# Performance work log

Measured on AMD Instinct MI355X. Metric: run time of the kernel, lower is better.

The kernel has to match this reference:

```python
import jax, jax.numpy as jnp
import numpy as np

HIDDEN = 2048
N_HEADS = 16
N_KV_HEADS = 4
HEAD_DIM = HIDDEN // N_HEADS  # 128
BATCH = 2
SEQ = 2048


def setup_inputs() -> dict:
    key = jax.random.key(0)
    ks = jax.random.split(key, 10)
    s = 0.02
    return {
        "hidden_states": jax.random.normal(ks[0], (BATCH, SEQ, HIDDEN), jnp.float32),
        "attention_mask": jnp.ones((BATCH, SEQ), jnp.int32),
        # weights stored [in, out] so y = x @ W + b (transpose of torch layout)
        "Wq": jax.random.normal(ks[1], (HIDDEN, N_HEADS * HEAD_DIM), jnp.float32) * s,
        "bq": jnp.zeros((N_HEADS * HEAD_DIM,), jnp.float32),
        "Wk": jax.random.normal(ks[2], (HIDDEN, N_KV_HEADS * HEAD_DIM), jnp.float32) * s,
        "bk": jnp.zeros((N_KV_HEADS * HEAD_DIM,), jnp.float32),
        "Wv": jax.random.normal(ks[3], (HIDDEN, N_KV_HEADS * HEAD_DIM), jnp.float32) * s,
        "bv": jnp.zeros((N_KV_HEADS * HEAD_DIM,), jnp.float32),
        "Wo": jax.random.normal(ks[4], (N_HEADS * HEAD_DIM, HIDDEN), jnp.float32) * s,
        "bo": jnp.zeros((HIDDEN,), jnp.float32),
    }


def reference(hidden_states, attention_mask, Wq, bq, Wk, bk, Wv, bv, Wo, bo):
    B, S, _ = hidden_states.shape
    q = hidden_states @ Wq + bq  # [B,S,H*D]
    k = hidden_states @ Wk + bk  # [B,S,Hkv*D]
    v = hidden_states @ Wv + bv

    q = q.reshape(B, S, N_HEADS, HEAD_DIM).transpose(0, 2, 1, 3)      # [B,H,S,D]
    k = k.reshape(B, S, N_KV_HEADS, HEAD_DIM).transpose(0, 2, 1, 3)   # [B,Hkv,S,D]
    v = v.reshape(B, S, N_KV_HEADS, HEAD_DIM).transpose(0, 2, 1, 3)

    # GQA: repeat_interleave along head dim (head h uses kv head h // groups)
    groups = N_HEADS // N_KV_HEADS
    k = jnp.repeat(k, groups, axis=1)  # [B,H,S,D]
    v = jnp.repeat(v, groups, axis=1)

    scale = 1.0 / np.sqrt(HEAD_DIM)
    scores = jnp.einsum('bhqd,bhkd->bhqk', q, k) * scale  # [B,H,S,S]

    causal = jnp.tril(jnp.ones((S, S), bool))              # True = keep
    keep = causal[None, None, :, :] & (attention_mask[:, None, None, :] != 0)
    scores = jnp.where(keep, scores, -jnp.inf)

    attn = jax.nn.softmax(scores.astype(jnp.float32), axis=-1).astype(q.dtype)
    out = jnp.einsum('bhqk,bhkd->bhqd', attn, v)            # [B,H,S,D]
    out = out.transpose(0, 2, 1, 3).reshape(B, S, N_HEADS * HEAD_DIM)
    return out @ Wo + bo
```

## Files before the change

### kernel.cpp

```cpp
#include <hip/hip_runtime.h>
#include <hip/hip_bf16.h>


typedef unsigned short u16;
typedef __attribute__((ext_vector_type(8))) short short8;
typedef __attribute__((ext_vector_type(4))) float f32x4;

#define BATCH 2
#define SEQ 2048
#define HIDDEN 2048
#define NH 16
#define NKV 4
#define HD 128
#define QKV_N 3072
#define MROWS 4096

__device__ inline u16 f2bf(float f) {
    __hip_bfloat16 h = __float2bfloat16(f);
    return __builtin_bit_cast(u16, h);
}

__device__ inline void async_copy16(const u16* g, u16* lds_base) {
    __builtin_amdgcn_global_load_lds(
        (const __attribute__((address_space(1))) void*)g,
        (__attribute__((address_space(3))) void*)lds_base, 16, 0, 0);
}

__global__ void convert_f32_bf16(const float* __restrict__ src, u16* __restrict__ dst, int n) {
    int i = (blockIdx.x * 256 + threadIdx.x) * 4;
    if (i + 3 < n) {
        float4 v = *(const float4*)(src + i);
        ushort4 o;
        o.x = f2bf(v.x); o.y = f2bf(v.y); o.z = f2bf(v.z); o.w = f2bf(v.w);
        *(ushort4*)(dst + i) = o;
    }
}

__global__ void transpose_f32_bf16(const float* __restrict__ src, u16* __restrict__ dst,
                                   int K, int N) {
    __shared__ float tile[32][33];
    int n0 = blockIdx.x * 32, k0 = blockIdx.y * 32;
    int tx = threadIdx.x, ty = threadIdx.y;
#pragma unroll
    for (int i = 0; i < 32; i += 8)
        tile[ty + i][tx] = src[(size_t)(k0 + ty + i) * N + n0 + tx];
    __syncthreads();
#pragma unroll
    for (int i = 0; i < 32; i += 8)
        dst[(size_t)(n0 + ty + i) * K + k0 + tx] = f2bf(tile[tx][ty + i]);
}

__global__ void build_bias(const float* __restrict__ bq, const float* __restrict__ bk,
                           const float* __restrict__ bv, float* __restrict__ bqkv) {
    int i = blockIdx.x * 256 + threadIdx.x;
    if (i < QKV_N)
        bqkv[i] = (i < 2048) ? bq[i] : ((i < 2560) ? bk[i - 2048] : bv[i - 2560]);
}

__global__ void vt_from_qkv(const u16* __restrict__ qkv, u16* __restrict__ vt) {
    __shared__ u16 tile[32][33];
    int b = blockIdx.z >> 2, kvh = blockIdx.z & 3;
    int s0 = blockIdx.x * 32, d0 = blockIdx.y * 32;
    int tx = threadIdx.x, ty = threadIdx.y;
#pragma unroll
    for (int i = 0; i < 32; i += 8)
        tile[ty + i][tx] = qkv[(size_t)(b * SEQ + s0 + ty + i) * QKV_N + 2560 + kvh * HD + d0 + tx];
    __syncthreads();
#pragma unroll
    for (int i = 0; i < 32; i += 8)
        vt[(size_t)((b * NKV + kvh) * HD + d0 + ty + i) * SEQ + s0 + tx] = tile[tx][ty + i];
}

template <bool OUT_BF16>
__global__ __launch_bounds__(256)
void gemm_bf16_128(const u16* __restrict__ A, const u16* __restrict__ BT,
                   const float* __restrict__ bias, void* __restrict__ outp,
                   int M, int N, int K) {
    __shared__ __align__(16) u16 As[128][32];
    __shared__ __align__(16) u16 Bs[128][32];
    int t = threadIdx.x, w = t >> 6, lane = t & 63, quad = lane >> 4, l16 = lane & 15;
    int wm = w & 1, wn = w >> 1;
    int bm0 = blockIdx.y * 128, bn0 = blockIdx.x * 128;

    f32x4 acc[4][4];
#pragma unroll
    for (int i = 0; i < 4; i++)
#pragma unroll
        for (int j = 0; j < 4; j++) acc[i][j] = (f32x4){0.f, 0.f, 0.f, 0.f};

    for (int k0 = 0; k0 < K; k0 += 32) {
        __syncthreads();
#pragma unroll
        for (int j = 0; j < 2; j++) {
            int f = (w * 2 + j) * 64 + lane;
            int row = f >> 2, col = (f & 3) * 8;
            u16* abase = &As[0][0] + (size_t)(w * 2 + j) * 512;
            u16* bbase = &Bs[0][0] + (size_t)(w * 2 + j) * 512;
            async_copy16(A + (size_t)(bm0 + row) * K + k0 + col, abase);
            async_copy16(BT + (size_t)(bn0 + row) * K + k0 + col, bbase);
        }
        __syncthreads();
        short8 af[4], bf[4];
#pragma unroll
        for (int mt = 0; mt < 4; mt++) af[mt] = *(const short8*)(&As[wm * 64 + mt * 16 + l16][quad * 8]);
#pragma unroll
        for (int nt = 0; nt < 4; nt++) bf[nt] = *(const short8*)(&Bs[wn * 64 + nt * 16 + l16][quad * 8]);
#pragma unroll
        for (int mt = 0; mt < 4; mt++)
#pragma unroll
            for (int nt = 0; nt < 4; nt++)
                acc[mt][nt] = __builtin_amdgcn_mfma_f32_16x16x32_bf16(af[mt], bf[nt], acc[mt][nt], 0, 0, 0);
    }
#pragma unroll
    for (int nt = 0; nt < 4; nt++) {
        int col = bn0 + wn * 64 + nt * 16 + l16;
        float bcol = bias[col];
#pragma unroll
        for (int mt = 0; mt < 4; mt++) {
#pragma unroll
            for (int r = 0; r < 4; r++) {
                int row = bm0 + wm * 64 + mt * 16 + quad * 4 + r;
                float v = acc[mt][nt][r] + bcol;
                if constexpr (OUT_BF16)
                    ((u16*)outp)[(size_t)row * N + col] = f2bf(v);
                else
                    ((float*)outp)[(size_t)row * N + col] = v;
            }
        }
    }
}

__global__ __launch_bounds__(512, 4)
void flash_attn(const u16* __restrict__ qkv, const u16* __restrict__ vt,
                const int* __restrict__ amask, u16* __restrict__ attn) {
    __shared__ __align__(16) u16 Ks[64][136];
    __shared__ __align__(16) u16 Vs[128][72];
    __shared__ __align__(16) u16 Pb[8][16][72];
    int t = threadIdx.x, w = t >> 6, lane = t & 63, quad = lane >> 4, l16 = lane & 15;
    int bx = blockIdx.x, b = blockIdx.z;
    int qt = b ? ((int)gridDim.x - 1 - bx) : bx;
    int h = blockIdx.y, kvh = h >> 2;
    int q_row0 = qt * 128 + w * 16;
    u16(*P)[72] = Pb[w];

    const u16* qrow = qkv + (size_t)(b * SEQ + q_row0 + l16) * QKV_N + h * HD;
    short8 qf[4];
#pragma unroll
    for (int c = 0; c < 4; c++) qf[c] = *(const short8*)(qrow + c * 32 + quad * 8);

    f32x4 o[8];
#pragma unroll
    for (int dt = 0; dt < 8; dt++) o[dt] = (f32x4){0.f, 0.f, 0.f, 0.f};
    float lpart[4] = {0.f, 0.f, 0.f, 0.f};

    const float scale2 = 0.12751743f;
    const float C2 = 14.4269504f;

    const u16* kgb = qkv + (size_t)(b * SEQ) * QKV_N + 2048 + kvh * HD;
    const u16* vgb = vt + (size_t)((b * NKV + kvh) * HD) * SEQ;
    const int* am = amask + b * SEQ;

    int kr = t >> 4, kc = (t & 15) * 8;
    int ksrc = 4 * (kr & 15) + (kr >> 4);
    int vr = t >> 3, vc = (t & 7) * 8;
    int kb_end = (qt + 1) * 128;

    short8 k0p, k1p, v0p, v1p;
    {
        k0p = *(const short8*)(kgb + (size_t)ksrc * QKV_N + kc);
        k1p = *(const short8*)(kgb + (size_t)(ksrc + 2) * QKV_N + kc);
        v0p = *(const short8*)(vgb + (size_t)vr * SEQ + vc);
        v1p = *(const short8*)(vgb + (size_t)(vr + 64) * SEQ + vc);
    }

    for (int kb = 0; kb < kb_end; kb += 64) {
        __syncthreads();
        *(short8*)(&Ks[kr][kc]) = k0p;
        *(short8*)(&Ks[kr + 32][kc]) = k1p;
        *(short8*)(&Vs[vr][vc]) = v0p;
        *(short8*)(&Vs[vr + 64][vc]) = v1p;
        __syncthreads();
        if (kb + 64 < kb_end) {
            const u16* kg = kgb + (size_t)(kb + 64) * QKV_N;
            const u16* vg = vgb + kb + 64;
            k0p = *(const short8*)(kg + (size_t)ksrc * QKV_N + kc);
            k1p = *(const short8*)(kg + (size_t)(ksrc + 2) * QKV_N + kc);
            v0p = *(const short8*)(vg + (size_t)vr * SEQ + vc);
            v1p = *(const short8*)(vg + (size_t)(vr + 64) * SEQ + vc);
        }
        if (kb > q_row0 + 15) continue;

        f32x4 sc[4];
#pragma unroll
        for (int nt = 0; nt < 4; nt++) sc[nt] = (f32x4){0.f, 0.f, 0.f, 0.f};
        __builtin_amdgcn_s_setprio(1);
#pragma unroll
        for (int c = 0; c < 4; c++) {
#pragma unroll
            for (int nt = 0; nt < 4; nt++) {
                short8 kf = *(const short8*)(&Ks[nt * 16 + l16][c * 32 + quad * 8]);
                sc[nt] = __builtin_amdgcn_mfma_f32_16x16x32_bf16(qf[c], kf, sc[nt], 0, 0, 0);
            }
        }
        __builtin_amdgcn_s_setprio(0);

        int kbase = kb + 4 * l16;
        int4 mk = *(const int4*)(am + kbase);
#pragma unroll
        for (int r = 0; r < 4; r++) {
            int qi = q_row0 + quad * 4 + r;
            float v0 = (mk.x && kbase     <= qi) ? sc[0][r] : -INFINITY;
            float v1 = (mk.y && kbase + 1 <= qi) ? sc[1][r] : -INFINITY;
            float v2 = (mk.z && kbase + 2 <= qi) ? sc[2][r] : -INFINITY;
            float v3 = (mk.w && kbase + 3 <= qi) ? sc[3][r] : -INFINITY;
            float p0 = __builtin_exp2f(__builtin_fmaf(v0, scale2, -C2));
            float p1 = __builtin_exp2f(__builtin_fmaf(v1, scale2, -C2));
            float p2 = __builtin_exp2f(__builtin_fmaf(v2, scale2, -C2));
            float p3 = __builtin_exp2f(__builtin_fmaf(v3, scale2, -C2));
            lpart[r] += (p0 + p1) + (p2 + p3);
            uint2 pk;
            pk.x = (unsigned)f2bf(p0) | ((unsigned)f2bf(p1) << 16);
            pk.y = (unsigned)f2bf(p2) | ((unsigned)f2bf(p3) << 16);
            *(uint2*)(&P[quad * 4 + r][4 * l16]) = pk;
        }
        short8 vf0[8];
#pragma unroll
        for (int dt = 0; dt < 8; dt++)
            vf0[dt] = *(const short8*)(&Vs[dt * 16 + l16][quad * 8]);
        asm volatile("s_waitcnt lgkmcnt(0)" ::: "memory");
        short8 pf0 = *(const short8*)(&P[l16][quad * 8]);
        short8 pf1 = *(const short8*)(&P[l16][32 + quad * 8]);
        __builtin_amdgcn_s_setprio(1);
#pragma unroll
        for (int dt = 0; dt < 8; dt++)
            o[dt] = __builtin_amdgcn_mfma_f32_16x16x32_bf16(pf0, vf0[dt], o[dt], 0, 0, 0);
#pragma unroll
        for (int dt = 0; dt < 8; dt++) {
            short8 vf1 = *(const short8*)(&Vs[dt * 16 + l16][32 + quad * 8]);
            o[dt] = __builtin_amdgcn_mfma_f32_16x16x32_bf16(pf1, vf1, o[dt], 0, 0, 0);
        }
        __builtin_amdgcn_s_setprio(0);
    }
    float inv[4];
#pragma unroll
    for (int r = 0; r < 4; r++) {
        float l = lpart[r];
#pragma unroll
        for (int off = 1; off < 16; off <<= 1) l += __shfl_xor(l, off, 64);
        inv[r] = l > 0.f ? 1.f / l : 0.f;
    }
    size_t obase = (size_t)(b * SEQ + q_row0) * HIDDEN + h * HD;
#pragma unroll
    for (int dt = 0; dt < 8; dt++)
#pragma unroll
        for (int r = 0; r < 4; r++)
            attn[obase + (size_t)(quad * 4 + r) * HIDDEN + dt * 16 + l16] = f2bf(o[dt][r] * inv[r]);
}

extern "C" void kernel_launch(void* const* d_in, const int* in_sizes, int n_in,
                              void* d_out, int out_size, void* d_ws, size_t ws_size,
                              hipStream_t stream) {
    const float* hidden = (const float*)d_in[0];
    const int* amask   = (const int*)d_in[1];
    const float* Wq = (const float*)d_in[2];
    const float* bq = (const float*)d_in[3];
    const float* Wk = (const float*)d_in[4];
    const float* bk = (const float*)d_in[5];
    const float* Wv = (const float*)d_in[6];
    const float* bv = (const float*)d_in[7];
    const float* Wo = (const float*)d_in[8];
    const float* bo = (const float*)d_in[9];
    float* out = (float*)d_out;

    char* ws = (char*)d_ws;
    u16* xb     = (u16*)ws;  ws += (size_t)MROWS * HIDDEN * 2;
    u16* wqkvT  = (u16*)ws;  ws += (size_t)QKV_N * HIDDEN * 2;
    u16* woT    = (u16*)ws;  ws += (size_t)HIDDEN * HIDDEN * 2;
    float* bqkv = (float*)ws; ws += (size_t)QKV_N * 4;
    u16* qkv    = (u16*)ws;  ws += (size_t)MROWS * QKV_N * 2;
    u16* vt     = (u16*)ws;  ws += (size_t)BATCH * NKV * HD * SEQ * 2;
    u16* attn   = (u16*)ws;  ws += (size_t)MROWS * HIDDEN * 2;

    convert_f32_bf16<<<dim3(MROWS * HIDDEN / 1024), dim3(256), 0, stream>>>(hidden, xb, MROWS * HIDDEN);
    transpose_f32_bf16<<<dim3(64, 64), dim3(32, 8), 0, stream>>>(Wq, wqkvT, HIDDEN, 2048);
    transpose_f32_bf16<<<dim3(16, 64), dim3(32, 8), 0, stream>>>(Wk, wqkvT + (size_t)2048 * HIDDEN, HIDDEN, 512);
    transpose_f32_bf16<<<dim3(16, 64), dim3(32, 8), 0, stream>>>(Wv, wqkvT + (size_t)2560 * HIDDEN, HIDDEN, 512);
    transpose_f32_bf16<<<dim3(64, 64), dim3(32, 8), 0, stream>>>(Wo, woT, HIDDEN, HIDDEN);
    build_bias<<<dim3(12), dim3(256), 0, stream>>>(bq, bk, bv, bqkv);

    gemm_bf16_128<true><<<dim3(QKV_N / 128, MROWS / 128), dim3(256), 0, stream>>>(
        xb, wqkvT, bqkv, qkv, MROWS, QKV_N, HIDDEN);

    vt_from_qkv<<<dim3(SEQ / 32, HD / 32, BATCH * NKV), dim3(32, 8), 0, stream>>>(qkv, vt);

    flash_attn<<<dim3(SEQ / 128, NH, BATCH), dim3(512), 0, stream>>>(qkv, vt, amask, attn);

    gemm_bf16_128<false><<<dim3(HIDDEN / 128, MROWS / 128), dim3(256), 0, stream>>>(
        attn, woT, bo, out, MROWS, HIDDEN, HIDDEN);
}
```

Baseline: 338.3 us.

## Process 32 query rows per wave in flash attention with 4-wave blocks

Each wave now handles two 16-row query groups instead of one, so the block shrinks to 256 threads while still covering 128 query rows. Every K and V fragment read from LDS feeds two MFMAs, halving LDS reads per unit of compute, and each thread loads four K/V vectors per tile instead of two. The cost is more registers per thread (doubled accumulators and Q fragments), lower occupancy bounds, and coarser causal skipping per wave.

Measured after the change: 345.6 us. 2.2% more time.

```diff
diff --git a/kernel.cpp b/kernel.cpp
--- a/kernel.cpp
+++ b/kernel.cpp
@@ -130,28 +130,33 @@
     }
 }
 
-__global__ __launch_bounds__(512, 4)
+__global__ __launch_bounds__(256, 2)
 void flash_attn(const u16* __restrict__ qkv, const u16* __restrict__ vt,
                 const int* __restrict__ amask, u16* __restrict__ attn) {
     __shared__ __align__(16) u16 Ks[64][136];
     __shared__ __align__(16) u16 Vs[128][72];
-    __shared__ __align__(16) u16 Pb[8][16][72];
+    __shared__ __align__(16) u16 Pb[4][32][72];
     int t = threadIdx.x, w = t >> 6, lane = t & 63, quad = lane >> 4, l16 = lane & 15;
     int bx = blockIdx.x, b = blockIdx.z;
     int qt = b ? ((int)gridDim.x - 1 - bx) : bx;
     int h = blockIdx.y, kvh = h >> 2;
-    int q_row0 = qt * 128 + w * 16;
+    int q_row0 = qt * 128 + w * 32;
     u16(*P)[72] = Pb[w];
 
-    const u16* qrow = qkv + (size_t)(b * SEQ + q_row0 + l16) * QKV_N + h * HD;
-    short8 qf[4];
-#pragma unroll
-    for (int c = 0; c < 4; c++) qf[c] = *(const short8*)(qrow + c * 32 + quad * 8);
-
-    f32x4 o[8];
-#pragma unroll
-    for (int dt = 0; dt < 8; dt++) o[dt] = (f32x4){0.f, 0.f, 0.f, 0.f};
-    float lpart[4] = {0.f, 0.f, 0.f, 0.f};
+    short8 qf[2][4];
+#pragma unroll
+    for (int g = 0; g < 2; g++) {
+        const u16* qrow = qkv + (size_t)(b * SEQ + q_row0 + g * 16 + l16) * QKV_N + h * HD;
+#pragma unroll
+        for (int c = 0; c < 4; c++) qf[g][c] = *(const short8*)(qrow + c * 32 + quad * 8);
+    }
+
+    f32x4 o[2][8];
+#pragma unroll
+    for (int g = 0; g < 2; g++)
+#pragma unroll
+        for (int dt = 0; dt < 8; dt++) o[g][dt] = (f32x4){0.f, 0.f, 0.f, 0.f};
+    float lpart[2][4] = {{0.f, 0.f, 0.f, 0.f}, {0.f, 0.f, 0.f, 0.f}};
 
     const float scale2 = 0.12751743f;
     const float C2 = 14.4269504f;
@@ -161,45 +166,49 @@
     const int* am = amask + b * SEQ;
 
     int kr = t >> 4, kc = (t & 15) * 8;
-    int ksrc = 4 * (kr & 15) + (kr >> 4);
+    int ksrc = 4 * kr;
     int vr = t >> 3, vc = (t & 7) * 8;
     int kb_end = (qt + 1) * 128;
 
-    short8 k0p, k1p, v0p, v1p;
-    {
-        k0p = *(const short8*)(kgb + (size_t)ksrc * QKV_N + kc);
-        k1p = *(const short8*)(kgb + (size_t)(ksrc + 2) * QKV_N + kc);
-        v0p = *(const short8*)(vgb + (size_t)vr * SEQ + vc);
-        v1p = *(const short8*)(vgb + (size_t)(vr + 64) * SEQ + vc);
+    short8 kp[4], vp[4];
+#pragma unroll
+    for (int j = 0; j < 4; j++) {
+        kp[j] = *(const short8*)(kgb + (size_t)(ksrc + j) * QKV_N + kc);
+        vp[j] = *(const short8*)(vgb + (size_t)(vr + 32 * j) * SEQ + vc);
     }
 
     for (int kb = 0; kb < kb_end; kb += 64) {
         __syncthreads();
-        *(short8*)(&Ks[kr][kc]) = k0p;
-        *(short8*)(&Ks[kr + 32][kc]) = k1p;
-        *(short8*)(&Vs[vr][vc]) = v0p;
-        *(short8*)(&Vs[vr + 64][vc]) = v1p;
+#pragma unroll
+        for (int j = 0; j < 4; j++) {
+            *(short8*)(&Ks[kr + 16 * j][kc]) = kp[j];
+            *(short8*)(&Vs[vr + 32 * j][vc]) = vp[j];
+        }
         __syncthreads();
         if (kb + 64 < kb_end) {
             const u16* kg = kgb + (size_t)(kb + 64) * QKV_N;
             const u16* vg = vgb + kb + 64;
-            k0p = *(const short8*)(kg + (size_t)ksrc * QKV_N + kc);
-            k1p = *(const short8*)(kg + (size_t)(ksrc + 2) * QKV_N + kc);
-            v0p = *(const short8*)(vg + (size_t)vr * SEQ + vc);
-            v1p = *(const short8*)(vg + (size_t)(vr + 64) * SEQ + vc);
-        }
-        if (kb > q_row0 + 15) continue;
-
-        f32x4 sc[4];
-#pragma unroll
-        for (int nt = 0; nt < 4; nt++) sc[nt] = (f32x4){0.f, 0.f, 0.f, 0.f};
+#pragma unroll
+            for (int j = 0; j < 4; j++) {
+                kp[j] = *(const short8*)(kg + (size_t)(ksrc + j) * QKV_N + kc);
+                vp[j] = *(const short8*)(vg + (size_t)(vr + 32 * j) * SEQ + vc);
+            }
+        }
+        if (kb > q_row0 + 31) continue;
+
+        f32x4 sc[2][4];
+#pragma unroll
+        for (int g = 0; g < 2; g++)
+#pragma unroll
+            for (int nt = 0; nt < 4; nt++) sc[g][nt] = (f32x4){0.f, 0.f, 0.f, 0.f};
         __builtin_amdgcn_s_setprio(1);
 #pragma unroll
         for (int c = 0; c < 4; c++) {
 #pragma unroll
             for (int nt = 0; nt < 4; nt++) {
                 short8 kf = *(const short8*)(&Ks[nt * 16 + l16][c * 32 + quad * 8]);
-                sc[nt] = __builtin_amdgcn_mfma_f32_16x16x32_bf16(qf[c], kf, sc[nt], 0, 0, 0);
+                sc[0][nt] = __builtin_amdgcn_mfma_f32_16x16x32_bf16(qf[0][c], kf, sc[0][nt], 0, 0, 0);
+                sc[1][nt] = __builtin_amdgcn_mfma_f32_16x16x32_bf16(qf[1][c], kf, sc[1][nt], 0, 0, 0);
             }
         }
         __builtin_amdgcn_s_setprio(0);
@@ -207,54 +216,74 @@
         int kbase = kb + 4 * l16;
         int4 mk = *(const int4*)(am + kbase);
 #pragma unroll
-        for (int r = 0; r < 4; r++) {
-            int qi = q_row0 + quad * 4 + r;
-            float v0 = (mk.x && kbase     <= qi) ? sc[0][r] : -INFINITY;
-            float v1 = (mk.y && kbase + 1 <= qi) ? sc[1][r] : -INFINITY;
-            float v2 = (mk.z && kbase + 2 <= qi) ? sc[2][r] : -INFINITY;
-            float v3 = (mk.w && kbase + 3 <= qi) ? sc[3][r] : -INFINITY;
-            float p0 = __builtin_exp2f(__builtin_fmaf(v0, scale2, -C2));
-            float p1 = __builtin_exp2f(__builtin_fmaf(v1, scale2, -C2));
-            float p2 = __builtin_exp2f(__builtin_fmaf(v2, scale2, -C2));
-            float p3 = __builtin_exp2f(__builtin_fmaf(v3, scale2, -C2));
-            lpart[r] += (p0 + p1) + (p2 + p3);
-            uint2 pk;
-            pk.x = (unsigned)f2bf(p0) | ((unsigned)f2bf(p1) << 16);
-            pk.y = (unsigned)f2bf(p2) | ((unsigned)f2bf(p3) << 16);
-            *(uint2*)(&P[quad * 4 + r][4 * l16]) = pk;
-        }
-        short8 vf0[8];
-#pragma unroll
-        for (int dt = 0; dt < 8; dt++)
-            vf0[dt] = *(const short8*)(&Vs[dt * 16 + l16][quad * 8]);
+        for (int g = 0; g < 2; g++) {
+#pragma unroll
+            for (int r = 0; r < 4; r++) {
+                int qi = q_row0 + g * 16 + quad * 4 + r;
+                float v0 = (mk.x && kbase     <= qi) ? sc[g][0][r] : -INFINITY;
+                float v1 = (mk.y && kbase + 1 <= qi) ? sc[g][1][r] : -INFINITY;
+                float v2 = (mk.z && kbase + 2 <= qi) ? sc[g][2][r] : -INFINITY;
+                float v3 = (mk.w && kbase + 3 <= qi) ? sc[g][3][r] : -INFINITY;
+                float p0 = __builtin_exp2f(__builtin_fmaf(v0, scale2, -C2));
+                float p1 = __builtin_exp2f(__builtin_fmaf(v1, scale2, -C2));
+                float p2 = __builtin_exp2f(__builtin_fmaf(v2, scale2, -C2));
+                float p3 = __builtin_exp2f(__builtin_fmaf(v3, scale2, -C2));
+                lpart[g][r] += (p0 + p1) + (p2 + p3);
+                uint2 pk;
+                pk.x = (unsigned)f2bf(p0) | ((unsigned)f2bf(p1) << 16);
+                pk.y = (unsigned)f2bf(p2) | ((unsigned)f2bf(p3) << 16);
+                *(uint2*)(&P[g * 16 + quad * 4 + r][4 * l16]) = pk;
+            }
+        }
+        short8 vf0a[4];
+#pragma unroll
+        for (int dt = 0; dt < 4; dt++)
+            vf0a[dt] = *(const short8*)(&Vs[dt * 16 + l16][quad * 8]);
         asm volatile("s_waitcnt lgkmcnt(0)" ::: "memory");
-        short8 pf0 = *(const short8*)(&P[l16][quad * 8]);
-        short8 pf1 = *(const short8*)(&P[l16][32 + quad * 8]);
+        short8 pf00 = *(const short8*)(&P[l16][quad * 8]);
+        short8 pf01 = *(const short8*)(&P[l16][32 + quad * 8]);
+        short8 pf10 = *(const short8*)(&P[16 + l16][quad * 8]);
+        short8 pf11 = *(const short8*)(&P[16 + l16][32 + quad * 8]);
         __builtin_amdgcn_s_setprio(1);
 #pragma unroll
-        for (int dt = 0; dt < 8; dt++)
-            o[dt] = __builtin_amdgcn_mfma_f32_16x16x32_bf16(pf0, vf0[dt], o[dt], 0, 0, 0);
+        for (int dt = 0; dt < 4; dt++) {
+            o[0][dt] = __builtin_amdgcn_mfma_f32_16x16x32_bf16(pf00, vf0a[dt], o[0][dt], 0, 0, 0);
+            o[1][dt] = __builtin_amdgcn_mfma_f32_16x16x32_bf16(pf10, vf0a[dt], o[1][dt], 0, 0, 0);
+        }
+#pragma unroll
+        for (int dt = 4; dt < 8; dt++) {
+            short8 vf0 = *(const short8*)(&Vs[dt * 16 + l16][quad * 8]);
+            o[0][dt] = __builtin_amdgcn_mfma_f32_16x16x32_bf16(pf00, vf0, o[0][dt], 0, 0, 0);
+            o[1][dt] = __builtin_amdgcn_mfma_f32_16x16x32_bf16(pf10, vf0, o[1][dt], 0, 0, 0);
+        }
 #pragma unroll
         for (int dt = 0; dt < 8; dt++) {
             short8 vf1 = *(const short8*)(&Vs[dt * 16 + l16][32 + quad * 8]);
-            o[dt] = __builtin_amdgcn_mfma_f32_16x16x32_bf16(pf1, vf1, o[dt], 0, 0, 0);
+            o[0][dt] = __builtin_amdgcn_mfma_f32_16x16x32_bf16(pf01, vf1, o[0][dt], 0, 0, 0);
+            o[1][dt] = __builtin_amdgcn_mfma_f32_16x16x32_bf16(pf11, vf1, o[1][dt], 0, 0, 0);
         }
         __builtin_amdgcn_s_setprio(0);
     }
-    float inv[4];
-#pragma unroll
-    for (int r = 0; r < 4; r++) {
-        float l = lpart[r];
-#pragma unroll
-        for (int off = 1; off < 16; off <<= 1) l += __shfl_xor(l, off, 64);
-        inv[r] = l > 0.f ? 1.f / l : 0.f;
-    }
-    size_t obase = (size_t)(b * SEQ + q_row0) * HIDDEN + h * HD;
-#pragma unroll
-    for (int dt = 0; dt < 8; dt++)
-#pragma unroll
-        for (int r = 0; r < 4; r++)
-            attn[obase + (size_t)(quad * 4 + r) * HIDDEN + dt * 16 + l16] = f2bf(o[dt][r] * inv[r]);
+    float inv[2][4];
+#pragma unroll
+    for (int g = 0; g < 2; g++)
+#pragma unroll
+        for (int r = 0; r < 4; r++) {
+            float l = lpart[g][r];
+#pragma unroll
+            for (int off = 1; off < 16; off <<= 1) l += __shfl_xor(l, off, 64);
+            inv[g][r] = l > 0.f ? 1.f / l : 0.f;
+        }
+#pragma unroll
+    for (int g = 0; g < 2; g++) {
+        size_t obase = (size_t)(b * SEQ + q_row0 + g * 16) * HIDDEN + h * HD;
+#pragma unroll
+        for (int dt = 0; dt < 8; dt++)
+#pragma unroll
+            for (int r = 0; r < 4; r++)
+                attn[obase + (size_t)(quad * 4 + r) * HIDDEN + dt * 16 + l16] =
+                    f2bf(o[g][dt][r] * inv[g][r]);
+    }
 }
 
 extern "C" void kernel_launch(void* const* d_in, const int* in_sizes, int n_in,
@@ -293,7 +322,7 @@
 
     vt_from_qkv<<<dim3(SEQ / 32, HD / 32, BATCH * NKV), dim3(32, 8), 0, stream>>>(qkv, vt);
 
-    flash_attn<<<dim3(SEQ / 128, NH, BATCH), dim3(512), 0, stream>>>(qkv, vt, amask, attn);
+    flash_attn<<<dim3(SEQ / 128, NH, BATCH), dim3(256), 0, stream>>>(qkv, vt, amask, attn);
 
     gemm_bf16_128<false><<<dim3(HIDDEN / 128, MROWS / 128), dim3(256), 0, stream>>>(
         attn, woT, bo, out, MROWS, HIDDEN, HIDDEN);
```

## Keep softmax probabilities in registers via permlane swaps instead of LDS round-trip

Applied to the files above, without the earlier changes.

The flash attention kernel now computes S^T by swapping MFMA operands, so each lane holds scores for one query row across keys. It converts probabilities with v_cvt_pk_bf16_f32 and rearranges them into the PV A-operand layout with permlane16/32 swaps, which removes the per-warp P buffer in LDS and its wait. The attention mask is pre-packed into 64-bit bitmasks by a new small kernel, replacing per-block int4 mask loads. The row-sum reduction and the K load order are simplified to match, which adds gfx950-specific inline asm and the risk of layout mistakes.

New measurement: 328.9 us. 2.8% less time.

```diff
diff --git a/kernel.cpp b/kernel.cpp
--- a/kernel.cpp
+++ b/kernel.cpp
@@ -3,8 +3,10 @@
 
 
 typedef unsigned short u16;
+typedef unsigned long long u64;
 typedef __attribute__((ext_vector_type(8))) short short8;
 typedef __attribute__((ext_vector_type(4))) float f32x4;
+typedef __attribute__((ext_vector_type(4))) unsigned uint4v;
 
 #define BATCH 2
 #define SEQ 2048
@@ -55,6 +57,21 @@
     int i = blockIdx.x * 256 + threadIdx.x;
     if (i < QKV_N)
         bqkv[i] = (i < 2048) ? bq[i] : ((i < 2560) ? bk[i - 2048] : bv[i - 2560]);
+}
+
+__global__ void pack_mask(const int* __restrict__ am, u64* __restrict__ mp) {
+    int i = blockIdx.x * 64 + threadIdx.x;
+    if (i < BATCH * SEQ / 64) {
+        const int* a = am + i * 64;
+        u64 m = 0;
+#pragma unroll
+        for (int j = 0; j < 64; j += 4) {
+            int4 v = *(const int4*)(a + j);
+            m |= ((u64)(v.x != 0) << j) | ((u64)(v.y != 0) << (j + 1)) |
+                 ((u64)(v.z != 0) << (j + 2)) | ((u64)(v.w != 0) << (j + 3));
+        }
+        mp[i] = m;
+    }
 }
 
 __global__ void vt_from_qkv(const u16* __restrict__ qkv, u16* __restrict__ vt) {
@@ -132,16 +149,14 @@
 
 __global__ __launch_bounds__(512, 4)
 void flash_attn(const u16* __restrict__ qkv, const u16* __restrict__ vt,
-                const int* __restrict__ amask, u16* __restrict__ attn) {
+                const u64* __restrict__ mp, u16* __restrict__ attn) {
     __shared__ __align__(16) u16 Ks[64][136];
     __shared__ __align__(16) u16 Vs[128][72];
-    __shared__ __align__(16) u16 Pb[8][16][72];
     int t = threadIdx.x, w = t >> 6, lane = t & 63, quad = lane >> 4, l16 = lane & 15;
     int bx = blockIdx.x, b = blockIdx.z;
     int qt = b ? ((int)gridDim.x - 1 - bx) : bx;
     int h = blockIdx.y, kvh = h >> 2;
     int q_row0 = qt * 128 + w * 16;
-    u16(*P)[72] = Pb[w];
 
     const u16* qrow = qkv + (size_t)(b * SEQ + q_row0 + l16) * QKV_N + h * HD;
     short8 qf[4];
@@ -151,24 +166,23 @@
     f32x4 o[8];
 #pragma unroll
     for (int dt = 0; dt < 8; dt++) o[dt] = (f32x4){0.f, 0.f, 0.f, 0.f};
-    float lpart[4] = {0.f, 0.f, 0.f, 0.f};
+    float lpart = 0.f;
 
     const float scale2 = 0.12751743f;
     const float C2 = 14.4269504f;
 
     const u16* kgb = qkv + (size_t)(b * SEQ) * QKV_N + 2048 + kvh * HD;
     const u16* vgb = vt + (size_t)((b * NKV + kvh) * HD) * SEQ;
-    const int* am = amask + b * SEQ;
+    const u64* mpb = mp + b * (SEQ / 64);
 
     int kr = t >> 4, kc = (t & 15) * 8;
-    int ksrc = 4 * (kr & 15) + (kr >> 4);
     int vr = t >> 3, vc = (t & 7) * 8;
     int kb_end = (qt + 1) * 128;
 
     short8 k0p, k1p, v0p, v1p;
     {
-        k0p = *(const short8*)(kgb + (size_t)ksrc * QKV_N + kc);
-        k1p = *(const short8*)(kgb + (size_t)(ksrc + 2) * QKV_N + kc);
+        k0p = *(const short8*)(kgb + (size_t)kr * QKV_N + kc);
+        k1p = *(const short8*)(kgb + (size_t)(kr + 32) * QKV_N + kc);
         v0p = *(const short8*)(vgb + (size_t)vr * SEQ + vc);
         v1p = *(const short8*)(vgb + (size_t)(vr + 64) * SEQ + vc);
     }
@@ -183,13 +197,15 @@
         if (kb + 64 < kb_end) {
             const u16* kg = kgb + (size_t)(kb + 64) * QKV_N;
             const u16* vg = vgb + kb + 64;
-            k0p = *(const short8*)(kg + (size_t)ksrc * QKV_N + kc);
-            k1p = *(const short8*)(kg + (size_t)(ksrc + 2) * QKV_N + kc);
+            k0p = *(const short8*)(kg + (size_t)kr * QKV_N + kc);
+            k1p = *(const short8*)(kg + (size_t)(kr + 32) * QKV_N + kc);
             v0p = *(const short8*)(vg + (size_t)vr * SEQ + vc);
             v1p = *(const short8*)(vg + (size_t)(vr + 64) * SEQ + vc);
         }
         if (kb > q_row0 + 15) continue;
 
+        u64 mk = mpb[kb >> 6];
+
         f32x4 sc[4];
 #pragma unroll
         for (int nt = 0; nt < 4; nt++) sc[nt] = (f32x4){0.f, 0.f, 0.f, 0.f};
@@ -199,41 +215,63 @@
 #pragma unroll
             for (int nt = 0; nt < 4; nt++) {
                 short8 kf = *(const short8*)(&Ks[nt * 16 + l16][c * 32 + quad * 8]);
-                sc[nt] = __builtin_amdgcn_mfma_f32_16x16x32_bf16(qf[c], kf, sc[nt], 0, 0, 0);
+                sc[nt] = __builtin_amdgcn_mfma_f32_16x16x32_bf16(kf, qf[c], sc[nt], 0, 0, 0);
             }
         }
         __builtin_amdgcn_s_setprio(0);
 
-        int kbase = kb + 4 * l16;
-        int4 mk = *(const int4*)(am + kbase);
-#pragma unroll
-        for (int r = 0; r < 4; r++) {
-            int qi = q_row0 + quad * 4 + r;
-            float v0 = (mk.x && kbase     <= qi) ? sc[0][r] : -INFINITY;
-            float v1 = (mk.y && kbase + 1 <= qi) ? sc[1][r] : -INFINITY;
-            float v2 = (mk.z && kbase + 2 <= qi) ? sc[2][r] : -INFINITY;
-            float v3 = (mk.w && kbase + 3 <= qi) ? sc[3][r] : -INFINITY;
-            float p0 = __builtin_exp2f(__builtin_fmaf(v0, scale2, -C2));
-            float p1 = __builtin_exp2f(__builtin_fmaf(v1, scale2, -C2));
-            float p2 = __builtin_exp2f(__builtin_fmaf(v2, scale2, -C2));
-            float p3 = __builtin_exp2f(__builtin_fmaf(v3, scale2, -C2));
-            lpart[r] += (p0 + p1) + (p2 + p3);
-            uint2 pk;
-            pk.x = (unsigned)f2bf(p0) | ((unsigned)f2bf(p1) << 16);
-            pk.y = (unsigned)f2bf(p2) | ((unsigned)f2bf(p3) << 16);
-            *(uint2*)(&P[quad * 4 + r][4 * l16]) = pk;
-        }
-        short8 vf0[8];
-#pragma unroll
-        for (int dt = 0; dt < 8; dt++)
-            vf0[dt] = *(const short8*)(&Vs[dt * 16 + l16][quad * 8]);
-        asm volatile("s_waitcnt lgkmcnt(0)" ::: "memory");
-        short8 pf0 = *(const short8*)(&P[l16][quad * 8]);
-        short8 pf1 = *(const short8*)(&P[l16][32 + quad * 8]);
+        short8 vf0a[4];
+#pragma unroll
+        for (int dt = 0; dt < 4; dt++)
+            vf0a[dt] = *(const short8*)(&Vs[dt * 16 + l16][quad * 8]);
+
+        int limit = q_row0 + l16 - kb;
+        float p[4][4];
+#pragma unroll
+        for (int nt = 0; nt < 4; nt++) {
+            unsigned nib = (unsigned)(mk >> (nt * 16 + quad * 4));
+#pragma unroll
+            for (int r = 0; r < 4; r++) {
+                int bp = nt * 16 + quad * 4 + r;
+                bool ok = ((nib >> r) & 1u) && (bp <= limit);
+                float v = ok ? sc[nt][r] : -INFINITY;
+                p[nt][r] = __builtin_exp2f(__builtin_fmaf(v, scale2, -C2));
+            }
+        }
+        lpart += ((p[0][0] + p[0][1]) + (p[0][2] + p[0][3])) +
+                 ((p[1][0] + p[1][1]) + (p[1][2] + p[1][3])) +
+                 ((p[2][0] + p[2][1]) + (p[2][2] + p[2][3])) +
+                 ((p[3][0] + p[3][1]) + (p[3][2] + p[3][3]));
+
+        unsigned A0, A1, B0, B1, C0, C1, E0, E1;
+        asm("v_cvt_pk_bf16_f32 %0, %1, %2" : "=v"(A0) : "v"(p[0][0]), "v"(p[0][1]));
+        asm("v_cvt_pk_bf16_f32 %0, %1, %2" : "=v"(A1) : "v"(p[0][2]), "v"(p[0][3]));
+        asm("v_cvt_pk_bf16_f32 %0, %1, %2" : "=v"(B0) : "v"(p[1][0]), "v"(p[1][1]));
+        asm("v_cvt_pk_bf16_f32 %0, %1, %2" : "=v"(B1) : "v"(p[1][2]), "v"(p[1][3]));
+        asm("v_cvt_pk_bf16_f32 %0, %1, %2" : "=v"(C0) : "v"(p[2][0]), "v"(p[2][1]));
+        asm("v_cvt_pk_bf16_f32 %0, %1, %2" : "=v"(C1) : "v"(p[2][2]), "v"(p[2][3]));
+        asm("v_cvt_pk_bf16_f32 %0, %1, %2" : "=v"(E0) : "v"(p[3][0]), "v"(p[3][1]));
+        asm("v_cvt_pk_bf16_f32 %0, %1, %2" : "=v"(E1) : "v"(p[3][2]), "v"(p[3][3]));
+        asm("v_permlane32_swap_b32 %0, %1" : "+v"(A0), "+v"(B0));
+        asm("v_permlane16_swap_b32 %0, %1" : "+v"(A0), "+v"(B0));
+        asm("v_permlane32_swap_b32 %0, %1" : "+v"(A1), "+v"(B1));
+        asm("v_permlane16_swap_b32 %0, %1" : "+v"(A1), "+v"(B1));
+        asm("v_permlane32_swap_b32 %0, %1" : "+v"(C0), "+v"(E0));
+        asm("v_permlane16_swap_b32 %0, %1" : "+v"(C0), "+v"(E0));
+        asm("v_permlane32_swap_b32 %0, %1" : "+v"(C1), "+v"(E1));
+        asm("v_permlane16_swap_b32 %0, %1" : "+v"(C1), "+v"(E1));
+        short8 pf0 = __builtin_bit_cast(short8, (uint4v){A0, A1, B0, B1});
+        short8 pf1 = __builtin_bit_cast(short8, (uint4v){C0, C1, E0, E1});
+
         __builtin_amdgcn_s_setprio(1);
 #pragma unroll
-        for (int dt = 0; dt < 8; dt++)
-            o[dt] = __builtin_amdgcn_mfma_f32_16x16x32_bf16(pf0, vf0[dt], o[dt], 0, 0, 0);
+        for (int dt = 0; dt < 4; dt++)
+            o[dt] = __builtin_amdgcn_mfma_f32_16x16x32_bf16(pf0, vf0a[dt], o[dt], 0, 0, 0);
+#pragma unroll
+        for (int dt = 4; dt < 8; dt++) {
+            short8 vf0 = *(const short8*)(&Vs[dt * 16 + l16][quad * 8]);
+            o[dt] = __builtin_amdgcn_mfma_f32_16x16x32_bf16(pf0, vf0, o[dt], 0, 0, 0);
+        }
 #pragma unroll
         for (int dt = 0; dt < 8; dt++) {
             short8 vf1 = *(const short8*)(&Vs[dt * 16 + l16][32 + quad * 8]);
@@ -241,20 +279,22 @@
         }
         __builtin_amdgcn_s_setprio(0);
     }
-    float inv[4];
+    float l = lpart;
+    l += __shfl_xor(l, 16, 64);
+    l += __shfl_xor(l, 32, 64);
+    float invq[4];
 #pragma unroll
     for (int r = 0; r < 4; r++) {
-        float l = lpart[r];
-#pragma unroll
-        for (int off = 1; off < 16; off <<= 1) l += __shfl_xor(l, off, 64);
-        inv[r] = l > 0.f ? 1.f / l : 0.f;
+        float lr = __shfl(l, quad * 4 + r, 16);
+        invq[r] = lr > 0.f ? 1.f / lr : 0.f;
     }
     size_t obase = (size_t)(b * SEQ + q_row0) * HIDDEN + h * HD;
 #pragma unroll
     for (int dt = 0; dt < 8; dt++)
 #pragma unroll
         for (int r = 0; r < 4; r++)
-            attn[obase + (size_t)(quad * 4 + r) * HIDDEN + dt * 16 + l16] = f2bf(o[dt][r] * inv[r]);
+            attn[obase + (size_t)(quad * 4 + r) * HIDDEN + dt * 16 + l16] =
+                f2bf(o[dt][r] * invq[r]);
 }
 
 extern "C" void kernel_launch(void* const* d_in, const int* in_sizes, int n_in,
@@ -277,6 +317,7 @@
     u16* wqkvT  = (u16*)ws;  ws += (size_t)QKV_N * HIDDEN * 2;
     u16* woT    = (u16*)ws;  ws += (size_t)HIDDEN * HIDDEN * 2;
     float* bqkv = (float*)ws; ws += (size_t)QKV_N * 4;
+    u64* mpk    = (u64*)ws;  ws += (size_t)(MROWS / 64) * 8;
     u16* qkv    = (u16*)ws;  ws += (size_t)MROWS * QKV_N * 2;
     u16* vt     = (u16*)ws;  ws += (size_t)BATCH * NKV * HD * SEQ * 2;
     u16* attn   = (u16*)ws;  ws += (size_t)MROWS * HIDDEN * 2;
@@ -287,13 +328,14 @@
     transpose_f32_bf16<<<dim3(16, 64), dim3(32, 8), 0, stream>>>(Wv, wqkvT + (size_t)2560 * HIDDEN, HIDDEN, 512);
     transpose_f32_bf16<<<dim3(64, 64), dim3(32, 8), 0, stream>>>(Wo, woT, HIDDEN, HIDDEN);
     build_bias<<<dim3(12), dim3(256), 0, stream>>>(bq, bk, bv, bqkv);
+    pack_mask<<<dim3(1), dim3(64), 0, stream>>>(amask, mpk);
 
     gemm_bf16_128<true><<<dim3(QKV_N / 128, MROWS / 128), dim3(256), 0, stream>>>(
         xb, wqkvT, bqkv, qkv, MROWS, QKV_N, HIDDEN);
 
     vt_from_qkv<<<dim3(SEQ / 32, HD / 32, BATCH * NKV), dim3(32, 8), 0, stream>>>(qkv, vt);
 
-    flash_attn<<<dim3(SEQ / 128, NH, BATCH), dim3(512), 0, stream>>>(qkv, vt, amask, attn);
+    flash_attn<<<dim3(SEQ / 128, NH, BATCH), dim3(512), 0, stream>>>(qkv, vt, mpk, attn);
 
     gemm_bf16_128<false><<<dim3(HIDDEN / 128, MROWS / 128), dim3(256), 0, stream>>>(
         attn, woT, bo, out, MROWS, HIDDEN, HIDDEN);
```
